# Optimization experiments

Hardware: AMD Instinct MI355X
Metric: run time of the kernel (lower is better)

Reference implementation:

```python
import jax, jax.numpy as jnp
import numpy as np

B, N = 128, 196
ENC, DEC, ATT = 2048, 512, 512

def setup_inputs() -> dict:
    key = jax.random.key(0)
    ks = jax.random.split(key, 8)
    s_enc = 1.0 / np.sqrt(ENC)
    s_dec = 1.0 / np.sqrt(DEC)
    s_att = 1.0 / np.sqrt(ATT)
    return {
        "encoder_out": jax.random.normal(ks[0], (B, N, ENC), jnp.float32),
        "decoder_hidden": jax.random.normal(ks[1], (B, DEC), jnp.float32),
        "W_enc": jax.random.uniform(ks[2], (ENC, ATT), jnp.float32, -s_enc, s_enc),
        "b_enc": jax.random.uniform(ks[3], (ATT,), jnp.float32, -s_enc, s_enc),
        "W_dec": jax.random.uniform(ks[4], (DEC, ATT), jnp.float32, -s_dec, s_dec),
        "b_dec": jax.random.uniform(ks[5], (ATT,), jnp.float32, -s_dec, s_dec),
        "W_full": jax.random.uniform(ks[6], (ATT,), jnp.float32, -s_att, s_att),
        "b_full": jax.random.uniform(ks[7], (), jnp.float32, -s_att, s_att),
    }

def reference(encoder_out, decoder_hidden, W_enc, b_enc, W_dec, b_dec, W_full, b_full):
    # att1: [B, N, ATT]; att2: [B, 1, ATT]
    att1 = jnp.einsum('bne,ea->bna', encoder_out, W_enc) + b_enc
    att2 = decoder_hidden @ W_dec + b_dec
    combined = jax.nn.relu(att1 + att2[:, None, :])
    e = jnp.einsum('bna,a->bn', combined, W_full) + b_full  # [B, N]
    alpha = jax.nn.softmax(e, axis=1)
    attention_weighted_encoding = jnp.einsum('bne,bn->be', encoder_out, alpha)
    return attention_weighted_encoding, alpha
```

## Files before the change

### kernel.cpp

```cpp
#include <hip/hip_runtime.h>
#include <hip/hip_bf16.h>

#define BB   128
#define NN   196
#define MM   (BB*NN)
#define ENC  2048
#define ATT  512
#define DEC  512

using f32x4 = __attribute__((ext_vector_type(4))) float;
using s16x8 = __attribute__((ext_vector_type(8))) short;

__device__ __forceinline__ short f2bf(float f) {
    union { __hip_bfloat16 h; short s; } u;
    u.h = __float2bfloat16(f);
    return u.s;
}

__global__ void transpose_convert_kernel(const float* __restrict__ W,
                                         unsigned short* __restrict__ Wt) {
    __shared__ float tile[32][33];
    const int a0 = blockIdx.x * 32;
    const int k0 = blockIdx.y * 32;
    const int tx = threadIdx.x & 31, ty = threadIdx.x >> 5;
    #pragma unroll
    for (int i = 0; i < 32; i += 8)
        tile[ty + i][tx] = W[(size_t)(k0 + ty + i) * ATT + a0 + tx];
    __syncthreads();
    #pragma unroll
    for (int i = 0; i < 32; i += 8) {
        union { __hip_bfloat16 h; unsigned short u; } v;
        v.h = __float2bfloat16(tile[tx][ty + i]);
        Wt[(size_t)(a0 + ty + i) * ENC + k0 + tx] = v.u;
    }
}

__global__ void att2_kernel(const float* __restrict__ dec,
                            const float* __restrict__ Wd,
                            const float* __restrict__ bd,
                            const float* __restrict__ benc,
                            float* __restrict__ att2) {
    const int b = blockIdx.x;
    const int t = threadIdx.x;
    __shared__ float sdec[DEC];
    sdec[t]       = dec[b * DEC + t];
    sdec[t + 256] = dec[b * DEC + t + 256];
    __syncthreads();
    float acc0 = bd[t] + benc[t];
    float acc1 = bd[t + 256] + benc[t + 256];
    #pragma unroll 8
    for (int k = 0; k < DEC; ++k) {
        float d = sdec[k];
        acc0 += d * Wd[k * ATT + t];
        acc1 += d * Wd[k * ATT + t + 256];
    }
    att2[b * ATT + t]       = acc0;
    att2[b * ATT + t + 256] = acc1;
}

__global__ __launch_bounds__(256, 3)
void gemm_e_kernel(const float* __restrict__ enc,
                   const unsigned short* __restrict__ Wt,
                   const float* __restrict__ att2,
                   const float* __restrict__ Wf,
                   float* __restrict__ e_part) {
    __shared__ float sA[64 * 32];
    __shared__ unsigned short sB[256 * 32];
    __shared__ float e_sm[64];

    const int t    = threadIdx.x;
    const int lane = t & 63;
    const int w    = t >> 6;
    const int aBlk  = blockIdx.x;
    const int mBase = blockIdx.y * 64;
    const int aBase = aBlk * 256;

    const char* gA[2];
    #pragma unroll
    for (int i = 0; i < 2; ++i) {
        int s = i * 256 + t;
        int row = s >> 3;
        int sc  = s & 7;
        int ck  = sc ^ (row & 7);
        gA[i] = (const char*)enc + ((size_t)(mBase + row) * ENC + (size_t)ck * 4) * 4;
    }
    const char* gB[4];
    #pragma unroll
    for (int i = 0; i < 4; ++i) {
        int s = i * 256 + t;
        int arow = s >> 2;
        int ck   = s & 3;
        gB[i] = (const char*)Wt + ((size_t)(aBase + arow) * ENC + (size_t)ck * 8) * 2;
    }
    char* lA = (char*)sA;
    char* lB = (char*)sB;

    const int r = lane & 15, q = lane >> 4;
    int offA[4][2];
    #pragma unroll
    for (int mi = 0; mi < 4; ++mi) {
        int lrow = mi * 16 + r;
        offA[mi][0] = lrow * 128 + (((2 * q)     ^ (lrow & 7)) * 16);
        offA[mi][1] = lrow * 128 + (((2 * q + 1) ^ (lrow & 7)) * 16);
    }
    int offB[4];
    #pragma unroll
    for (int ni = 0; ni < 4; ++ni) {
        int col = w * 64 + ni * 16 + r;
        offB[ni] = col * 64 + q * 16;
    }

    f32x4 acc[4][4] = {};

    for (int ks = 0; ks < ENC / 32; ++ks) {
        #pragma unroll
        for (int i = 0; i < 2; ++i)
            __builtin_amdgcn_global_load_lds(
                (const __attribute__((address_space(1))) void*)(gA[i] + (size_t)ks * 128),
                (__attribute__((address_space(3))) void*)(lA + (i * 256 + w * 64) * 16),
                16, 0, 0);
        #pragma unroll
        for (int i = 0; i < 4; ++i)
            __builtin_amdgcn_global_load_lds(
                (const __attribute__((address_space(1))) void*)(gB[i] + (size_t)ks * 64),
                (__attribute__((address_space(3))) void*)(lB + (i * 256 + w * 64) * 16),
                16, 0, 0);
        __syncthreads();

        s16x8 af[4], bf[4];
        #pragma unroll
        for (int mi = 0; mi < 4; ++mi) {
            f32x4 f0 = *(const f32x4*)((const char*)sA + offA[mi][0]);
            f32x4 f1 = *(const f32x4*)((const char*)sA + offA[mi][1]);
            s16x8 a;
            a[0] = f2bf(f0[0]); a[1] = f2bf(f0[1]); a[2] = f2bf(f0[2]); a[3] = f2bf(f0[3]);
            a[4] = f2bf(f1[0]); a[5] = f2bf(f1[1]); a[6] = f2bf(f1[2]); a[7] = f2bf(f1[3]);
            af[mi] = a;
        }
        #pragma unroll
        for (int ni = 0; ni < 4; ++ni)
            bf[ni] = *(const s16x8*)((const char*)sB + offB[ni]);

        #pragma unroll
        for (int mi = 0; mi < 4; ++mi)
            #pragma unroll
            for (int ni = 0; ni < 4; ++ni)
                acc[mi][ni] = __builtin_amdgcn_mfma_f32_16x16x32_bf16(
                    af[mi], bf[ni], acc[mi][ni], 0, 0, 0);
        __syncthreads();
    }

    if (t < 64) e_sm[t] = 0.f;
    __syncthreads();

    float wfv[4];
    #pragma unroll
    for (int ni = 0; ni < 4; ++ni)
        wfv[ni] = Wf[aBase + w * 64 + ni * 16 + r];

    #pragma unroll
    for (int mi = 0; mi < 4; ++mi) {
        #pragma unroll
        for (int reg = 0; reg < 4; ++reg) {
            int lrow = mi * 16 + q * 4 + reg;
            int gm = mBase + lrow;
            int b = gm / NN;
            const float* a2 = att2 + b * ATT + aBase + w * 64;
            float rs = 0.f;
            #pragma unroll
            for (int ni = 0; ni < 4; ++ni) {
                float v = acc[mi][ni][reg] + a2[ni * 16 + r];
                rs += fmaxf(v, 0.f) * wfv[ni];
            }
            atomicAdd(&e_sm[lrow], rs);
        }
    }
    __syncthreads();
    if (t < 64)
        e_part[(size_t)aBlk * MM + mBase + t] = e_sm[t];
}

__global__ void softmax_awe_kernel(const float* __restrict__ enc,
                                   const float* __restrict__ e_part,
                                   const float* __restrict__ b_full,
                                   float* __restrict__ out) {
    const int b = blockIdx.x;
    const int chunk = blockIdx.y;
    const int t = threadIdx.x;
    __shared__ float sm[256];
    __shared__ float alpha_sm[NN];

    float v = -3.0e38f;
    if (t < NN) {
        int gm = b * NN + t;
        v = e_part[gm] + e_part[MM + gm] + b_full[0];
    }
    sm[t] = v;
    __syncthreads();
    for (int s = 128; s > 0; s >>= 1) {
        if (t < s) sm[t] = fmaxf(sm[t], sm[t + s]);
        __syncthreads();
    }
    float mx = sm[0];
    __syncthreads();
    float ex = (t < NN) ? __expf(v - mx) : 0.f;
    sm[t] = ex;
    __syncthreads();
    for (int s = 128; s > 0; s >>= 1) {
        if (t < s) sm[t] += sm[t + s];
        __syncthreads();
    }
    float inv = 1.0f / sm[0];
    if (t < NN) alpha_sm[t] = ex * inv;
    __syncthreads();

    if (chunk == 0 && t < NN)
        out[BB * ENC + b * NN + t] = ex * inv;

    const int col = chunk * 256 + t;
    const float* ep = enc + (size_t)b * NN * ENC + col;
    float acc = 0.f;
    #pragma unroll 4
    for (int n = 0; n < NN; n += 4) {
        acc += ep[(size_t)n * ENC]       * alpha_sm[n]
             + ep[(size_t)(n + 1) * ENC] * alpha_sm[n + 1]
             + ep[(size_t)(n + 2) * ENC] * alpha_sm[n + 2]
             + ep[(size_t)(n + 3) * ENC] * alpha_sm[n + 3];
    }
    out[b * ENC + col] = acc;
}

extern "C" void kernel_launch(void* const* d_in, const int* in_sizes, int n_in,
                              void* d_out, int out_size, void* d_ws, size_t ws_size,
                              hipStream_t stream) {
    const float* enc    = (const float*)d_in[0];
    const float* dec    = (const float*)d_in[1];
    const float* W_enc  = (const float*)d_in[2];
    const float* b_enc  = (const float*)d_in[3];
    const float* W_dec  = (const float*)d_in[4];
    const float* b_dec  = (const float*)d_in[5];
    const float* W_full = (const float*)d_in[6];
    const float* b_full = (const float*)d_in[7];
    float* out = (float*)d_out;

    char* ws = (char*)d_ws;
    unsigned short* Wt = (unsigned short*)ws;
    float* att2   = (float*)(ws + (size_t)ENC * ATT * 2);
    float* e_part = (float*)(ws + (size_t)ENC * ATT * 2 + BB * ATT * 4);

    transpose_convert_kernel<<<dim3(ATT / 32, ENC / 32), 256, 0, stream>>>(W_enc, Wt);
    att2_kernel<<<BB, 256, 0, stream>>>(dec, W_dec, b_dec, b_enc, att2);
    gemm_e_kernel<<<dim3(2, MM / 64), 256, 0, stream>>>(enc, Wt, att2, W_full, e_part);
    softmax_awe_kernel<<<dim3(BB, 8), 256, 0, stream>>>(enc, e_part, b_full, out);
}
```

Before: 482.3 us.

## Load GEMM fragments directly from global into registers with double buffering

The encoder GEMM no longer stages A and B tiles through LDS with two barriers per k-step. Each lane now loads its MFMA fragments straight from global memory into registers, using two register buffers so the next k-step's loads are issued while the current one computes. Launch bounds drop to 2 waves per SIMD to make room for the extra registers. Separately, att2 is split over 8 column blocks with a 4-way k reduction in shared memory for more parallelism. The risks are that loads become uncoalesced, since each lane reads 32-byte runs from separate rows, and that data the LDS used to share across waves is now reloaded from cache.

Result: slower. 621.8 us (+28.9%).

```diff
diff --git a/kernel.cpp b/kernel.cpp
--- a/kernel.cpp
+++ b/kernel.cpp
@@ -40,32 +40,70 @@
                             const float* __restrict__ bd,
                             const float* __restrict__ benc,
                             float* __restrict__ att2) {
-    const int b = blockIdx.x;
-    const int t = threadIdx.x;
+    const int b  = blockIdx.x;
+    const int c0 = blockIdx.y * 64;
+    const int t  = threadIdx.x;
+    const int cl = t & 63, kg = t >> 6;
     __shared__ float sdec[DEC];
+    __shared__ float red[4][64];
     sdec[t]       = dec[b * DEC + t];
     sdec[t + 256] = dec[b * DEC + t + 256];
     __syncthreads();
-    float acc0 = bd[t] + benc[t];
-    float acc1 = bd[t + 256] + benc[t + 256];
+    float acc = 0.f;
+    const float* wp = Wd + c0 + cl;
     #pragma unroll 8
-    for (int k = 0; k < DEC; ++k) {
-        float d = sdec[k];
-        acc0 += d * Wd[k * ATT + t];
-        acc1 += d * Wd[k * ATT + t + 256];
-    }
-    att2[b * ATT + t]       = acc0;
-    att2[b * ATT + t + 256] = acc1;
-}
-
-__global__ __launch_bounds__(256, 3)
+    for (int k = kg * 128; k < kg * 128 + 128; ++k)
+        acc += sdec[k] * wp[(size_t)k * ATT];
+    red[kg][cl] = acc;
+    __syncthreads();
+    if (t < 64) {
+        float s = red[0][t] + red[1][t] + red[2][t] + red[3][t];
+        att2[b * ATT + c0 + t] = s + bd[c0 + t] + benc[c0 + t];
+    }
+}
+
+__device__ __forceinline__ void load_frags(const float* const pA[4],
+                                           const unsigned short* const pB[4],
+                                           int kk, f32x4 Af[4][2], s16x8 Bf[4]) {
+    #pragma unroll
+    for (int mi = 0; mi < 4; ++mi) {
+        const float* p = pA[mi] + (size_t)kk * 32;
+        Af[mi][0] = *(const f32x4*)p;
+        Af[mi][1] = *(const f32x4*)(p + 4);
+    }
+    #pragma unroll
+    for (int ni = 0; ni < 4; ++ni)
+        Bf[ni] = *(const s16x8*)(pB[ni] + (size_t)kk * 32);
+}
+
+__device__ __forceinline__ void compute_frags(const f32x4 Af[4][2],
+                                              const s16x8 Bf[4],
+                                              f32x4 acc[4][4]) {
+    s16x8 af[4];
+    #pragma unroll
+    for (int mi = 0; mi < 4; ++mi) {
+        s16x8 a;
+        #pragma unroll
+        for (int j = 0; j < 4; ++j) {
+            a[j]     = f2bf(Af[mi][0][j]);
+            a[4 + j] = f2bf(Af[mi][1][j]);
+        }
+        af[mi] = a;
+    }
+    #pragma unroll
+    for (int mi = 0; mi < 4; ++mi)
+        #pragma unroll
+        for (int ni = 0; ni < 4; ++ni)
+            acc[mi][ni] = __builtin_amdgcn_mfma_f32_16x16x32_bf16(
+                af[mi], Bf[ni], acc[mi][ni], 0, 0, 0);
+}
+
+__global__ __launch_bounds__(256, 2)
 void gemm_e_kernel(const float* __restrict__ enc,
                    const unsigned short* __restrict__ Wt,
                    const float* __restrict__ att2,
                    const float* __restrict__ Wf,
                    float* __restrict__ e_part) {
-    __shared__ float sA[64 * 32];
-    __shared__ unsigned short sB[256 * 32];
     __shared__ float e_sm[64];
 
     const int t    = threadIdx.x;
@@ -75,79 +113,29 @@
     const int mBase = blockIdx.y * 64;
     const int aBase = aBlk * 256;
 
-    const char* gA[2];
-    #pragma unroll
-    for (int i = 0; i < 2; ++i) {
-        int s = i * 256 + t;
-        int row = s >> 3;
-        int sc  = s & 7;
-        int ck  = sc ^ (row & 7);
-        gA[i] = (const char*)enc + ((size_t)(mBase + row) * ENC + (size_t)ck * 4) * 4;
-    }
-    const char* gB[4];
-    #pragma unroll
-    for (int i = 0; i < 4; ++i) {
-        int s = i * 256 + t;
-        int arow = s >> 2;
-        int ck   = s & 3;
-        gB[i] = (const char*)Wt + ((size_t)(aBase + arow) * ENC + (size_t)ck * 8) * 2;
-    }
-    char* lA = (char*)sA;
-    char* lB = (char*)sB;
-
     const int r = lane & 15, q = lane >> 4;
-    int offA[4][2];
-    #pragma unroll
-    for (int mi = 0; mi < 4; ++mi) {
-        int lrow = mi * 16 + r;
-        offA[mi][0] = lrow * 128 + (((2 * q)     ^ (lrow & 7)) * 16);
-        offA[mi][1] = lrow * 128 + (((2 * q + 1) ^ (lrow & 7)) * 16);
-    }
-    int offB[4];
-    #pragma unroll
-    for (int ni = 0; ni < 4; ++ni) {
-        int col = w * 64 + ni * 16 + r;
-        offB[ni] = col * 64 + q * 16;
-    }
+
+    const float* pA[4];
+    #pragma unroll
+    for (int mi = 0; mi < 4; ++mi)
+        pA[mi] = enc + (size_t)(mBase + mi * 16 + r) * ENC + q * 8;
+    const unsigned short* pB[4];
+    #pragma unroll
+    for (int ni = 0; ni < 4; ++ni)
+        pB[ni] = Wt + (size_t)(aBase + w * 64 + ni * 16 + r) * ENC + q * 8;
 
     f32x4 acc[4][4] = {};
-
-    for (int ks = 0; ks < ENC / 32; ++ks) {
-        #pragma unroll
-        for (int i = 0; i < 2; ++i)
-            __builtin_amdgcn_global_load_lds(
-                (const __attribute__((address_space(1))) void*)(gA[i] + (size_t)ks * 128),
-                (__attribute__((address_space(3))) void*)(lA + (i * 256 + w * 64) * 16),
-                16, 0, 0);
-        #pragma unroll
-        for (int i = 0; i < 4; ++i)
-            __builtin_amdgcn_global_load_lds(
-                (const __attribute__((address_space(1))) void*)(gB[i] + (size_t)ks * 64),
-                (__attribute__((address_space(3))) void*)(lB + (i * 256 + w * 64) * 16),
-                16, 0, 0);
-        __syncthreads();
-
-        s16x8 af[4], bf[4];
-        #pragma unroll
-        for (int mi = 0; mi < 4; ++mi) {
-            f32x4 f0 = *(const f32x4*)((const char*)sA + offA[mi][0]);
-            f32x4 f1 = *(const f32x4*)((const char*)sA + offA[mi][1]);
-            s16x8 a;
-            a[0] = f2bf(f0[0]); a[1] = f2bf(f0[1]); a[2] = f2bf(f0[2]); a[3] = f2bf(f0[3]);
-            a[4] = f2bf(f1[0]); a[5] = f2bf(f1[1]); a[6] = f2bf(f1[2]); a[7] = f2bf(f1[3]);
-            af[mi] = a;
-        }
-        #pragma unroll
-        for (int ni = 0; ni < 4; ++ni)
-            bf[ni] = *(const s16x8*)((const char*)sB + offB[ni]);
-
-        #pragma unroll
-        for (int mi = 0; mi < 4; ++mi)
-            #pragma unroll
-            for (int ni = 0; ni < 4; ++ni)
-                acc[mi][ni] = __builtin_amdgcn_mfma_f32_16x16x32_bf16(
-                    af[mi], bf[ni], acc[mi][ni], 0, 0, 0);
-        __syncthreads();
+    f32x4 A0[4][2], A1[4][2];
+    s16x8 B0[4], B1[4];
+
+    load_frags(pA, pB, 0, A0, B0);
+    #pragma unroll 1
+    for (int ks = 0; ks < ENC / 32; ks += 2) {
+        load_frags(pA, pB, ks + 1, A1, B1);
+        compute_frags(A0, B0, acc);
+        int kn = (ks + 2 < ENC / 32) ? ks + 2 : (ENC / 32 - 1);
+        load_frags(pA, pB, kn, A0, B0);
+        compute_frags(A1, B1, acc);
     }
 
     if (t < 64) e_sm[t] = 0.f;
@@ -249,7 +237,7 @@
     float* e_part = (float*)(ws + (size_t)ENC * ATT * 2 + BB * ATT * 4);
 
     transpose_convert_kernel<<<dim3(ATT / 32, ENC / 32), 256, 0, stream>>>(W_enc, Wt);
-    att2_kernel<<<BB, 256, 0, stream>>>(dec, W_dec, b_dec, b_enc, att2);
+    att2_kernel<<<dim3(BB, 8), 256, 0, stream>>>(dec, W_dec, b_dec, b_enc, att2);
     gemm_e_kernel<<<dim3(2, MM / 64), 256, 0, stream>>>(enc, Wt, att2, W_full, e_part);
     softmax_awe_kernel<<<dim3(BB, 8), 256, 0, stream>>>(enc, e_part, b_full, out);
 }
```
